# Kernel tuning notes

Measured on AMD Instinct MI355X. Metric: run time of the kernel, lower is better.

The kernel has to match this reference:

```python
import jax, jax.numpy as jnp
import numpy as np

B, N, D, H = 2, 2048, 1024, 16
HD = D // H  # 64
EPS = 1e-6


def setup_inputs() -> dict:
    key = jax.random.key(0)
    ks = jax.random.split(key, 16)
    rnd = lambda k, shp: jax.random.normal(k, shp, dtype=jnp.float32)
    w = lambda k, i, o: rnd(k, (i, o)) * 0.02  # stored as (in, out); y = x @ W
    return {
        "x": rnd(ks[0], (B, N, D)),
        "emb_B_D": rnd(ks[1], (B, D)),
        "gate": rnd(ks[2], (B, D)),
        "crossattn_emb": rnd(ks[3], (B, 128, D)),
        "rope_emb_L_1_1_D": rnd(ks[4], (N, HD)),
        "Wq1": w(ks[5], D, D), "Wq2": w(ks[6], D, D),
        "Wk1": w(ks[7], D, D), "Wk2": w(ks[8], D, D),
        "Wv": w(ks[9], D, D),
        "Wo": w(ks[10], D, D),
        "Wada1": w(ks[11], D, D),
        "Wada2": w(ks[12], D, 2 * D),
        "bada2": jnp.zeros((2 * D,), dtype=jnp.float32),
    }


def rotate_half(t):
    t1, t2 = jnp.split(t, 2, axis=-1)
    return jnp.concatenate([-t2, t1], axis=-1)


def reference(x, emb_B_D, gate, crossattn_emb, rope_emb_L_1_1_D,
              Wq1, Wq2, Wk1, Wk2, Wv, Wo, Wada1, Wada2, bada2):
    # adaLN modulation: SiLU -> Linear(no bias) -> Linear(bias)
    ada = jax.nn.silu(emb_B_D) @ Wada1 @ Wada2 + bada2          # [B, 2D]
    shift, scale = jnp.split(ada, 2, axis=1)                    # [B, D] each

    # LayerNorm (no affine) + scale/shift
    mu = jnp.mean(x, axis=-1, keepdims=True)
    var = jnp.var(x, axis=-1, keepdims=True)
    xn = (x - mu) * jax.lax.rsqrt(var + EPS)
    xn = xn * (1.0 + scale[:, None, :]) + shift[:, None, :]     # [B, N, D]

    # QKV projections (each to_q/to_k is two stacked linears, to_v one)
    q = xn @ Wq1 @ Wq2
    k = xn @ Wk1 @ Wk2
    v = xn @ Wv
    split_heads = lambda t: t.reshape(B, N, H, HD).transpose(0, 2, 1, 3)  # b h n d
    q, k, v = split_heads(q), split_heads(k), split_heads(v)

    # RoPE
    cos = jnp.cos(rope_emb_L_1_1_D)[None, None]                 # [1,1,N,HD]
    sin = jnp.sin(rope_emb_L_1_1_D)[None, None]
    q = q * cos + rotate_half(q) * sin
    k = k * cos + rotate_half(k) * sin

    # Attention
    sim = jnp.einsum("bhid,bhjd->bhij", q, k) * (HD ** -0.5)
    attn = jax.nn.softmax(sim, axis=-1)
    out = jnp.einsum("bhij,bhjd->bhid", attn, v)
    out = out.transpose(0, 2, 1, 3).reshape(B, N, D) @ Wo

    # Gated residual
    return x + gate[:, None, :] * out
```

## Files before the change

kernel.cpp:

```cpp
#include <hip/hip_runtime.h>
#include <stdint.h>
#include <math.h>

typedef unsigned short u16;
typedef __attribute__((ext_vector_type(8))) short short8;
typedef __attribute__((ext_vector_type(4))) float f32x4;
typedef __attribute__((ext_vector_type(4))) unsigned short u16x4;
typedef __attribute__((ext_vector_type(2))) unsigned int uint2v;

#define DEV static __device__ __forceinline__

DEV u16 f2bf(float f) {
    unsigned u = __builtin_bit_cast(unsigned, f);
    u = u + 0x7fffu + ((u >> 16) & 1u);
    return (u16)(u >> 16);
}
DEV float bf2f(u16 s) { return __builtin_bit_cast(float, ((unsigned)s) << 16); }
DEV unsigned pk2(float a, float b) {
    unsigned ua = __builtin_bit_cast(unsigned, a) + 0x8000u;
    unsigned ub = __builtin_bit_cast(unsigned, b) + 0x8000u;
    return (ua >> 16) | (ub & 0xffff0000u);
}
DEV float fexp2(float x) {
#if __has_builtin(__builtin_amdgcn_exp2f)
    return __builtin_amdgcn_exp2f(x);
#else
    return __expf(x * 0.69314718056f);
#endif
}

DEV void gl_lds16(const u16* g, u16* l) {
#if __has_builtin(__builtin_amdgcn_global_load_lds)
    __builtin_amdgcn_global_load_lds((const __attribute__((address_space(1))) unsigned int*)g,
                                     (__attribute__((address_space(3))) unsigned int*)l, 16, 0, 0);
#else
    *(short8*)l = *(const short8*)g;
#endif
}


__global__ __launch_bounds__(256) void k_ada1(const float* __restrict__ emb, const float* __restrict__ W,
                                              float* __restrict__ out) {
    int col = blockIdx.x * 64 + (threadIdx.x & 63);
    int b = blockIdx.y;
    int kbase = blockIdx.z * 128 + (threadIdx.x >> 6) * 32;
    float acc = 0.f;
    for (int k = kbase; k < kbase + 32; k++) {
        float e = emb[b * 1024 + k];
        float se = e / (1.f + __expf(-e));
        acc += se * W[(size_t)k * 1024 + col];
    }
    __shared__ float red[4][64];
    red[threadIdx.x >> 6][threadIdx.x & 63] = acc;
    __syncthreads();
    if (threadIdx.x < 64)
        atomicAdd(out + b * 1024 + blockIdx.x * 64 + threadIdx.x,
                  red[0][threadIdx.x] + red[1][threadIdx.x] + red[2][threadIdx.x] + red[3][threadIdx.x]);
}

__global__ __launch_bounds__(256) void k_prep(const float* s0, u16* d0, const float* s1, u16* d1,
                                              const float* s2, u16* d2, const float* s3, u16* d3,
                                              const float* s4, u16* d4, const float* s5, u16* d5,
                                              const float* __restrict__ t_ada, const float* __restrict__ Wada2,
                                              float* __restrict__ ada, const float* __restrict__ rope,
                                              float* __restrict__ cst, float* __restrict__ snt) {
    __shared__ u16 tile[64][65];
    __shared__ float red[4][64];
    if (blockIdx.z == 6) {
        int flat = blockIdx.y * 16 + blockIdx.x;
        int kq = flat >> 6;
        int rest = flat & 63;
        int b = rest >> 5, xb = rest & 31;
        int col = xb * 64 + (threadIdx.x & 63);
        int kbase = kq * 256 + (threadIdx.x >> 6) * 64;
        float acc = 0.f;
        for (int k = kbase; k < kbase + 64; k++)
            acc += t_ada[b * 1024 + k] * Wada2[(size_t)k * 2048 + col];
        red[threadIdx.x >> 6][threadIdx.x & 63] = acc;
        __syncthreads();
        if (threadIdx.x < 64)
            atomicAdd(ada + b * 2048 + xb * 64 + threadIdx.x,
                      red[0][threadIdx.x] + red[1][threadIdx.x] + red[2][threadIdx.x] + red[3][threadIdx.x]);
        return;
    }
    if (blockIdx.z == 7) {
        int flat = blockIdx.y * 16 + blockIdx.x;
        if (flat < 128) {
            int idx = flat * 1024 + threadIdx.x * 4;
            float4 rv = *(const float4*)(rope + idx);
            float4 cv, sv;
            __sincosf(rv.x, &sv.x, &cv.x);
            __sincosf(rv.y, &sv.y, &cv.y);
            __sincosf(rv.z, &sv.z, &cv.z);
            __sincosf(rv.w, &sv.w, &cv.w);
            *(float4*)(cst + idx) = cv;
            *(float4*)(snt + idx) = sv;
        }
        return;
    }
    const float* s; u16* d;
    switch (blockIdx.z) {
        case 0: s = s0; d = d0; break;
        case 1: s = s1; d = d1; break;
        case 2: s = s2; d = d2; break;
        case 3: s = s3; d = d3; break;
        case 4: s = s4; d = d4; break;
        default: s = s5; d = d5; break;
    }
    int k0 = blockIdx.x * 64, n0 = blockIdx.y * 64;
    int tx = threadIdx.x & 63, ty = threadIdx.x >> 6;
    if (blockIdx.z >= 4) {
        #pragma unroll
        for (int i = 0; i < 16; i++) {
            int kk = ty + 4 * i;
            d[(size_t)(k0 + kk) * 1024 + n0 + tx] = f2bf(s[(size_t)(k0 + kk) * 1024 + n0 + tx]);
        }
        return;
    }
    #pragma unroll
    for (int i = 0; i < 16; i++) {
        int kk = ty + 4 * i;
        tile[kk][tx] = f2bf(s[(size_t)(k0 + kk) * 1024 + n0 + tx]);
    }
    __syncthreads();
    #pragma unroll
    for (int i = 0; i < 16; i++) {
        int nn = ty + 4 * i;
        d[(size_t)(n0 + nn) * 1024 + k0 + tx] = tile[tx][nn];
    }
}

__global__ __launch_bounds__(256) void k_ln(const float* __restrict__ x, const float* __restrict__ ada,
                                            const float* __restrict__ bada2, u16* __restrict__ xn) {
    int row = blockIdx.x;
    int b = row >> 11;
    float4 v = ((const float4*)(x + (size_t)row * 1024))[threadIdx.x];
    float s = v.x + v.y + v.z + v.w;
    float ss = v.x * v.x + v.y * v.y + v.z * v.z + v.w * v.w;
    #pragma unroll
    for (int m = 1; m < 64; m <<= 1) { s += __shfl_xor(s, m, 64); ss += __shfl_xor(ss, m, 64); }
    __shared__ float red[2][4];
    int wave = threadIdx.x >> 6, lane = threadIdx.x & 63;
    if (lane == 0) { red[0][wave] = s; red[1][wave] = ss; }
    __syncthreads();
    s = red[0][0] + red[0][1] + red[0][2] + red[0][3];
    ss = red[1][0] + red[1][1] + red[1][2] + red[1][3];
    float mu = s * (1.f / 1024.f);
    float var = ss * (1.f / 1024.f) - mu * mu;
    float rs = rsqrtf(var + 1e-6f);
    int c = threadIdx.x * 4;
    const float* sh = ada + b * 2048;
    const float* sc = ada + b * 2048 + 1024;
    u16x4 r;
    r.x = f2bf((v.x - mu) * rs * (1.f + sc[c + 0] + bada2[1024 + c + 0]) + sh[c + 0] + bada2[c + 0]);
    r.y = f2bf((v.y - mu) * rs * (1.f + sc[c + 1] + bada2[1024 + c + 1]) + sh[c + 1] + bada2[c + 1]);
    r.z = f2bf((v.z - mu) * rs * (1.f + sc[c + 2] + bada2[1024 + c + 2]) + sh[c + 2] + bada2[c + 2]);
    r.w = f2bf((v.w - mu) * rs * (1.f + sc[c + 3] + bada2[1024 + c + 3]) + sh[c + 3] + bada2[c + 3]);
    *(u16x4*)(xn + (size_t)row * 1024 + c) = r;
}

template <int BM, int BN, int MODE>
DEV void gemm_core(const u16* __restrict__ A, const u16* __restrict__ Bt,
                   u16* __restrict__ Cb, float* __restrict__ Cf, u16* __restrict__ Vt,
                   const float* __restrict__ Xres, const float* __restrict__ gate,
                   const float* __restrict__ cst, const float* __restrict__ snt,
                   float scale, int Nn, int K, int m0, int n0) {
    constexpr int MI = BM / 32, NJ = BN / 32;
    constexpr int PA = BM / 64, PB = BN / 64;
    constexpr int LA = BM * 40, LB = BN * 40;
    __shared__ u16 smem[2 * (LA + LB)];
    int tid = threadIdx.x;
    int lane = tid & 63, wave = tid >> 6;
    int wm = (wave & 1) * (BM / 2), wn = (wave >> 1) * (BN / 2);
    int lr = lane & 15, quad = lane >> 4;
    f32x4 acc[MI][NJ];
    #pragma unroll
    for (int i = 0; i < MI; i++)
        #pragma unroll
        for (int j = 0; j < NJ; j++) acc[i][j] = f32x4{0.f, 0.f, 0.f, 0.f};

    int arow = tid >> 2;
    int achunk = (tid & 3) * 8;
    const u16* ap = A + (size_t)(m0 + arow) * K + achunk;
    const u16* bp = Bt + (size_t)(n0 + arow) * K + achunk;
    u16* AsL[2] = { smem, smem + LA };
    u16* BsL[2] = { smem + 2 * LA, smem + 2 * LA + LB };

    short8 ra[2][PA], rb[2][PB];
    #pragma unroll
    for (int p = 0; p < PA; p++) ra[0][p] = *(const short8*)(ap + (size_t)(64 * p) * K);
    #pragma unroll
    for (int p = 0; p < PB; p++) rb[0][p] = *(const short8*)(bp + (size_t)(64 * p) * K);
    #pragma unroll
    for (int p = 0; p < PA; p++) *(short8*)(&AsL[0][(arow + 64 * p) * 40 + achunk]) = ra[0][p];
    #pragma unroll
    for (int p = 0; p < PB; p++) *(short8*)(&BsL[0][(arow + 64 * p) * 40 + achunk]) = rb[0][p];
    #pragma unroll
    for (int p = 0; p < PA; p++) ra[1][p] = *(const short8*)(ap + 32 + (size_t)(64 * p) * K);
    #pragma unroll
    for (int p = 0; p < PB; p++) rb[1][p] = *(const short8*)(bp + 32 + (size_t)(64 * p) * K);
    __syncthreads();

    auto body = [&](int it, int cur) {
        if (it + 2 < 32) {
            int koff = (it + 2) * 32;
            #pragma unroll
            for (int p = 0; p < PA; p++) ra[cur][p] = *(const short8*)(ap + koff + (size_t)(64 * p) * K);
            #pragma unroll
            for (int p = 0; p < PB; p++) rb[cur][p] = *(const short8*)(bp + koff + (size_t)(64 * p) * K);
        }
        short8 af[MI], bfr[NJ];
        #pragma unroll
        for (int i = 0; i < MI; i++) af[i] = *(const short8*)(&AsL[cur][(wm + i * 16 + lr) * 40 + quad * 8]);
        #pragma unroll
        for (int j = 0; j < NJ; j++) bfr[j] = *(const short8*)(&BsL[cur][(wn + j * 16 + lr) * 40 + quad * 8]);
        #pragma unroll
        for (int i = 0; i < MI; i++)
            #pragma unroll
            for (int j = 0; j < NJ; j++)
                acc[i][j] = __builtin_amdgcn_mfma_f32_16x16x32_bf16(af[i], bfr[j], acc[i][j], 0, 0, 0);
        if (it + 1 < 32) {
            int nxt = cur ^ 1;
            #pragma unroll
            for (int p = 0; p < PA; p++) *(short8*)(&AsL[nxt][(arow + 64 * p) * 40 + achunk]) = ra[nxt][p];
            #pragma unroll
            for (int p = 0; p < PB; p++) *(short8*)(&BsL[nxt][(arow + 64 * p) * 40 + achunk]) = rb[nxt][p];
        }
        __syncthreads();
    };
    #pragma unroll 1
    for (int it2 = 0; it2 < 16; ++it2) {
        body(2 * it2, 0);
        body(2 * it2 + 1, 1);
    }

    if (MODE == 2) {
        if ((n0 + wn) < 2048) {
            #pragma unroll
            for (int i = 0; i < MI; i++)
                #pragma unroll
                for (int jp = 0; jp < 2; jp++)
                    #pragma unroll
                    for (int r = 0; r < 4; r++) {
                        int row = m0 + wm + i * 16 + quad * 4 + r;
                        int n = row & 2047;
                        int d1 = jp * 16 + lr;
                        float c1 = cst[n * 64 + d1],      s1 = snt[n * 64 + d1];
                        float c2 = cst[n * 64 + d1 + 32], s2 = snt[n * 64 + d1 + 32];
                        float x1 = acc[i][jp][r], x2 = acc[i][jp + 2][r];
                        Cb[(size_t)row * Nn + n0 + wn + d1]      = f2bf(x1 * c1 - x2 * s1);
                        Cb[(size_t)row * Nn + n0 + wn + d1 + 32] = f2bf(x2 * c2 + x1 * s2);
                    }
        } else {
            #pragma unroll
            for (int i = 0; i < MI; i++)
                #pragma unroll
                for (int j = 0; j < NJ; j++) {
                    u16x4 w;
                    w.x = f2bf(acc[i][j][0]); w.y = f2bf(acc[i][j][1]);
                    w.z = f2bf(acc[i][j][2]); w.w = f2bf(acc[i][j][3]);
                    *(u16x4*)(&smem[(wn + j * 16 + lr) * 132 + wm + i * 16 + quad * 4]) = w;
                }
            __syncthreads();
            int d = tid >> 1, half = tid & 1;
            int gcol = n0 - 2048 + d;
            int hv = gcol >> 6, dl = gcol & 63;
            int bb = m0 >> 11;
            int nloc = (m0 & 2047) + half * 64;
            u16* dst = Vt + ((size_t)((bb * 16 + hv) * 64 + dl)) * 2048 + nloc;
            #pragma unroll
            for (int c = 0; c < 8; c++)
                *(short8*)(dst + c * 8) = *(const short8*)(&smem[d * 132 + half * 64 + c * 8]);
        }
        return;
    }
    #pragma unroll
    for (int i = 0; i < MI; i++)
        #pragma unroll
        for (int j = 0; j < NJ; j++)
            #pragma unroll
            for (int r = 0; r < 4; r++) {
                int row = m0 + wm + i * 16 + quad * 4 + r;
                int col = n0 + wn + j * 16 + lr;
                float v = acc[i][j][r];
                if (MODE == 1) {
                    int b = row >> 11;
                    Cf[(size_t)row * Nn + col] = Xres[(size_t)row * Nn + col] + gate[b * 1024 + col] * v;
                } else {
                    Cb[(size_t)row * Nn + col] = f2bf(v * scale);
                }
            }
}

template <int BM, int BN, int MODE, int WPE>
__global__ __launch_bounds__(256, WPE) void gemm_bt(const u16* __restrict__ A, const u16* __restrict__ Bt,
                                                    u16* __restrict__ Cb, float* __restrict__ Cf,
                                                    u16* __restrict__ Vt,
                                                    const float* __restrict__ Xres, const float* __restrict__ gate,
                                                    const float* __restrict__ cst, const float* __restrict__ snt,
                                                    int Nn, int K) {
    gemm_core<BM, BN, MODE>(A, Bt, Cb, Cf, Vt, Xres, gate, cst, snt, 1.f, Nn, K,
                            blockIdx.y * BM, blockIdx.x * BN);
}

__global__ __launch_bounds__(256, 4) void gemm_fold(const u16* A0, const u16* B0, u16* C0,
                                                    const u16* A1, const u16* B1, u16* C1) {
    const u16* A = blockIdx.z ? A1 : A0;
    const u16* Bt = blockIdx.z ? B1 : B0;
    u16* C = blockIdx.z ? C1 : C0;
    float scale = blockIdx.z ? 1.0f : 0.18033688f;
    gemm_core<128, 64, 0>(A, Bt, C, nullptr, nullptr, nullptr, nullptr, nullptr, nullptr, scale,
                          1024, 1024, blockIdx.y * 128, blockIdx.x * 64);
}

__global__ __launch_bounds__(256) void k_attn(const u16* __restrict__ qkv, const u16* __restrict__ vt,
                                              u16* __restrict__ aob) {
    __shared__ u16 pool[128 * 72];
    __shared__ u16 Ks[2][64][64];
    __shared__ u16 Vs[2][64][64];
    int q0 = blockIdx.x * 128;
    int bh = blockIdx.y; int b = bh >> 4, h = bh & 15;
    int tid = threadIdx.x;
    int lane = tid & 63, wave = tid >> 6;
    int lr = lane & 15, quad = lane >> 4;
    int srow = tid >> 3, scol = (tid & 7) * 8;
    int sg = (((tid & 7) ^ (srow & 7))) * 8;
    int cc[2] = { ((quad ^ (lr & 7))) * 8, (((4 + quad) ^ (lr & 7))) * 8 };

    const u16* kp = qkv + ((size_t)(b * 2048 + srow)) * 2048 + 1024 + h * 64 + sg;
    const u16* vp = vt + ((size_t)(bh * 64 + srow)) * 2048 + sg;

    #pragma unroll
    for (int p = 0; p < 4; p++)
        gl_lds16(qkv + ((size_t)(b * 2048 + q0 + srow + 32 * p)) * 2048 + h * 64 + sg,
                 pool + (srow + 32 * p) * 64 + scol);

    short8 krA[2], vrA[2], krB[2], vrB[2];
    krA[0] = *(const short8*)(kp);               krA[1] = *(const short8*)(kp + (size_t)32 * 2048);
    vrA[0] = *(const short8*)(vp);               vrA[1] = *(const short8*)(vp + (size_t)32 * 2048);
    __syncthreads();
    short8 qf[2][2];
    #pragma unroll
    for (int rt = 0; rt < 2; rt++)
        #pragma unroll
        for (int ks = 0; ks < 2; ks++)
            qf[rt][ks] = *(const short8*)(pool + (wave * 32 + rt * 16 + lr) * 64 + cc[ks]);
    *(short8*)(&Ks[0][srow][scol])      = krA[0];
    *(short8*)(&Ks[0][srow + 32][scol]) = krA[1];
    *(short8*)(&Vs[0][srow][scol])      = vrA[0];
    *(short8*)(&Vs[0][srow + 32][scol]) = vrA[1];
    krB[0] = *(const short8*)(kp + (size_t)64 * 2048);  krB[1] = *(const short8*)(kp + (size_t)96 * 2048);
    vrB[0] = *(const short8*)(vp + 64);                 vrB[1] = *(const short8*)(vp + 64 + (size_t)32 * 2048);
    __syncthreads();

    float l_part[2] = {0.f, 0.f};
    f32x4 oacc[2][4];
    #pragma unroll
    for (int rt = 0; rt < 2; rt++)
        #pragma unroll
        for (int dt = 0; dt < 4; dt++) oacc[rt][dt] = f32x4{0.f, 0.f, 0.f, 0.f};

    auto body = [&](int it, int cur, short8 (&krF)[2], short8 (&vrF)[2],
                    short8 (&krH)[2], short8 (&vrH)[2]) {
        if (it < 30) {
            const u16* kq = kp + (size_t)(it + 2) * 64 * 2048;
            const u16* vq = vp + (it + 2) * 64;
            krF[0] = *(const short8*)(kq);  krF[1] = *(const short8*)(kq + (size_t)32 * 2048);
            vrF[0] = *(const short8*)(vq);  vrF[1] = *(const short8*)(vq + (size_t)32 * 2048);
        }
        f32x4 st[2][4];
        #pragma unroll
        for (int rt = 0; rt < 2; rt++)
            #pragma unroll
            for (int ct = 0; ct < 4; ct++) st[rt][ct] = f32x4{0.f, 0.f, 0.f, 0.f};
        #pragma unroll
        for (int ks = 0; ks < 2; ks++) {
            short8 kf[4];
            #pragma unroll
            for (int ct = 0; ct < 4; ct++)
                kf[ct] = *(const short8*)(&Ks[cur][ct * 16 + lr][cc[ks]]);
            __builtin_amdgcn_s_setprio(1);
            #pragma unroll
            for (int rt = 0; rt < 2; rt++)
                #pragma unroll
                for (int ct = 0; ct < 4; ct++)
                    st[rt][ct] = __builtin_amdgcn_mfma_f32_16x16x32_bf16(kf[ct], qf[rt][ks], st[rt][ct], 0, 0, 0);
            __builtin_amdgcn_s_setprio(0);
        }
        #pragma unroll
        for (int rt = 0; rt < 2; rt++)
            #pragma unroll
            for (int ct = 0; ct < 4; ct++) {
                float p0 = fexp2(st[rt][ct][0]);
                float p1 = fexp2(st[rt][ct][1]);
                float p2 = fexp2(st[rt][ct][2]);
                float p3 = fexp2(st[rt][ct][3]);
                l_part[rt] += (p0 + p1) + (p2 + p3);
                uint2v w; w.x = pk2(p0, p1); w.y = pk2(p2, p3);
                *(uint2v*)(pool + (wave * 32 + rt * 16 + lr) * 72 + ct * 16 + quad * 4) = w;
            }
        #pragma unroll
        for (int ks = 0; ks < 2; ks++) {
            short8 pf[2], vf[4];
            #pragma unroll
            for (int rt = 0; rt < 2; rt++)
                pf[rt] = *(const short8*)(pool + (wave * 32 + rt * 16 + lr) * 72 + ks * 32 + quad * 8);
            #pragma unroll
            for (int dt = 0; dt < 4; dt++)
                vf[dt] = *(const short8*)(&Vs[cur][dt * 16 + lr][cc[ks]]);
            __builtin_amdgcn_s_setprio(1);
            #pragma unroll
            for (int rt = 0; rt < 2; rt++)
                #pragma unroll
                for (int dt = 0; dt < 4; dt++)
                    oacc[rt][dt] = __builtin_amdgcn_mfma_f32_16x16x32_bf16(pf[rt], vf[dt], oacc[rt][dt], 0, 0, 0);
            __builtin_amdgcn_s_setprio(0);
        }
        if (it < 31) {
            int nxt = cur ^ 1;
            *(short8*)(&Ks[nxt][srow][scol])      = krH[0];
            *(short8*)(&Ks[nxt][srow + 32][scol]) = krH[1];
            *(short8*)(&Vs[nxt][srow][scol])      = vrH[0];
            *(short8*)(&Vs[nxt][srow + 32][scol]) = vrH[1];
        }
        __syncthreads();
    };

    #pragma unroll 1
    for (int it2 = 0; it2 < 16; ++it2) {
        body(2 * it2,     0, krA, vrA, krB, vrB);
        body(2 * it2 + 1, 1, krB, vrB, krA, vrA);
    }

    float linv[2][4];
    #pragma unroll
    for (int rt = 0; rt < 2; rt++) {
        float l = l_part[rt];
        l += __shfl_xor(l, 16, 64);
        l += __shfl_xor(l, 32, 64);
        #pragma unroll
        for (int r = 0; r < 4; r++)
            linv[rt][r] = 1.f / __shfl(l, quad * 4 + r, 64);
    }
    #pragma unroll
    for (int rt = 0; rt < 2; rt++)
        #pragma unroll
        for (int dt = 0; dt < 4; dt++)
            #pragma unroll
            for (int r = 0; r < 4; r++) {
                int row = q0 + wave * 32 + rt * 16 + quad * 4 + r;
                aob[((size_t)(b * 2048 + row)) * 1024 + h * 64 + dt * 16 + lr] =
                    f2bf(oacc[rt][dt][r] * linv[rt][r]);
            }
}

extern "C" void kernel_launch(void* const* d_in, const int* in_sizes, int n_in,
                              void* d_out, int out_size, void* d_ws, size_t ws_size,
                              hipStream_t stream) {
    const float* x     = (const float*)d_in[0];
    const float* emb   = (const float*)d_in[1];
    const float* gate  = (const float*)d_in[2];
    const float* rope  = (const float*)d_in[4];
    const float* Wq1   = (const float*)d_in[5];
    const float* Wq2   = (const float*)d_in[6];
    const float* Wk1   = (const float*)d_in[7];
    const float* Wk2   = (const float*)d_in[8];
    const float* Wv    = (const float*)d_in[9];
    const float* Wo    = (const float*)d_in[10];
    const float* Wada1 = (const float*)d_in[11];
    const float* Wada2 = (const float*)d_in[12];
    const float* bada2 = (const float*)d_in[13];
    float* out = (float*)d_out;

    char* ws = (char*)d_ws;
    size_t off = 0;
    auto alloc = [&](size_t bytes) { void* p = ws + off; off += (bytes + 255) & ~(size_t)255; return p; };
    float* t_ada = (float*)alloc(2048 * 4);
    float* ada   = (float*)alloc(4096 * 4);
    float* cst   = (float*)alloc((size_t)131072 * 4);
    float* snt   = (float*)alloc((size_t)131072 * 4);
    u16* xn    = (u16*)alloc((size_t)4096 * 1024 * 2);
    u16* Wq1b  = (u16*)alloc((size_t)1024 * 1024 * 2);
    u16* Wk1b  = (u16*)alloc((size_t)1024 * 1024 * 2);
    u16* Wq2t  = (u16*)alloc((size_t)1024 * 1024 * 2);
    u16* Wk2t  = (u16*)alloc((size_t)1024 * 1024 * 2);
    u16* Wot   = (u16*)alloc((size_t)1024 * 1024 * 2);
    u16* WqkvT = (u16*)alloc((size_t)3072 * 1024 * 2);
    u16* qkvb  = (u16*)alloc((size_t)4096 * 2048 * 2);
    u16* vtb   = (u16*)alloc((size_t)4096 * 1024 * 2);
    u16* aob   = (u16*)alloc((size_t)4096 * 1024 * 2);
    (void)ws_size; (void)in_sizes; (void)n_in; (void)out_size;

    hipMemsetAsync(t_ada, 0, 2048 * 4, stream);
    hipMemsetAsync(ada, 0, 4096 * 4, stream);

    k_ada1<<<dim3(16, 2, 8), 256, 0, stream>>>(emb, Wada1, t_ada);

    k_prep<<<dim3(16, 16, 8), 256, 0, stream>>>(Wq2, Wq2t, Wk2, Wk2t,
                                                Wv, WqkvT + (size_t)2048 * 1024, Wo, Wot,
                                                Wq1, Wq1b, Wk1, Wk1b,
                                                t_ada, Wada2, ada, rope, cst, snt);

    k_ln<<<4096, 256, 0, stream>>>(x, ada, bada2, xn);

    gemm_fold<<<dim3(16, 8, 2), 256, 0, stream>>>(Wq2t, Wq1b, WqkvT,
                                                  Wk2t, Wk1b, WqkvT + (size_t)1024 * 1024);

    gemm_bt<128, 128, 2, 3><<<dim3(24, 32), 256, 0, stream>>>(xn, WqkvT, qkvb, nullptr, vtb,
                                                              nullptr, nullptr, cst, snt, 2048, 1024);

    k_attn<<<dim3(16, 32), 256, 0, stream>>>(qkvb, vtb, aob);

    gemm_bt<128, 64, 1, 4><<<dim3(16, 32), 256, 0, stream>>>(aob, Wot, nullptr, out, nullptr, x, gate,
                                                             nullptr, nullptr, 1024, 1024);
}
```

Measured before the change: 265.1 us.

## Use 8 waves per attention block with 16 query rows per wave

The attention kernel now launches 512 threads per block instead of 256. Each wave handles 16 query rows rather than 32, and each thread loads one K/V chunk per tile instead of two. This raises the number of waves per block and cuts per-thread register use, which should help hide latency. In exchange, each K/V tile staged in LDS is reused by fewer rows per wave, and more threads take part in every block barrier.

```diff
diff --git a/kernel.cpp b/kernel.cpp
--- a/kernel.cpp
+++ b/kernel.cpp
@@ -313,7 +313,7 @@
                           1024, 1024, blockIdx.y * 128, blockIdx.x * 64);
 }
 
-__global__ __launch_bounds__(256) void k_attn(const u16* __restrict__ qkv, const u16* __restrict__ vt,
+__global__ __launch_bounds__(512) void k_attn(const u16* __restrict__ qkv, const u16* __restrict__ vt,
                                               u16* __restrict__ aob) {
     __shared__ u16 pool[128 * 72];
     __shared__ u16 Ks[2][64][64];
@@ -326,53 +326,43 @@
     int srow = tid >> 3, scol = (tid & 7) * 8;
     int sg = (((tid & 7) ^ (srow & 7))) * 8;
     int cc[2] = { ((quad ^ (lr & 7))) * 8, (((4 + quad) ^ (lr & 7))) * 8 };
+    int qrow = wave * 16 + lr;
 
     const u16* kp = qkv + ((size_t)(b * 2048 + srow)) * 2048 + 1024 + h * 64 + sg;
     const u16* vp = vt + ((size_t)(bh * 64 + srow)) * 2048 + sg;
 
     #pragma unroll
-    for (int p = 0; p < 4; p++)
-        gl_lds16(qkv + ((size_t)(b * 2048 + q0 + srow + 32 * p)) * 2048 + h * 64 + sg,
-                 pool + (srow + 32 * p) * 64 + scol);
-
-    short8 krA[2], vrA[2], krB[2], vrB[2];
-    krA[0] = *(const short8*)(kp);               krA[1] = *(const short8*)(kp + (size_t)32 * 2048);
-    vrA[0] = *(const short8*)(vp);               vrA[1] = *(const short8*)(vp + (size_t)32 * 2048);
-    __syncthreads();
-    short8 qf[2][2];
-    #pragma unroll
-    for (int rt = 0; rt < 2; rt++)
-        #pragma unroll
-        for (int ks = 0; ks < 2; ks++)
-            qf[rt][ks] = *(const short8*)(pool + (wave * 32 + rt * 16 + lr) * 64 + cc[ks]);
-    *(short8*)(&Ks[0][srow][scol])      = krA[0];
-    *(short8*)(&Ks[0][srow + 32][scol]) = krA[1];
-    *(short8*)(&Vs[0][srow][scol])      = vrA[0];
-    *(short8*)(&Vs[0][srow + 32][scol]) = vrA[1];
-    krB[0] = *(const short8*)(kp + (size_t)64 * 2048);  krB[1] = *(const short8*)(kp + (size_t)96 * 2048);
-    vrB[0] = *(const short8*)(vp + 64);                 vrB[1] = *(const short8*)(vp + 64 + (size_t)32 * 2048);
-    __syncthreads();
-
-    float l_part[2] = {0.f, 0.f};
-    f32x4 oacc[2][4];
-    #pragma unroll
-    for (int rt = 0; rt < 2; rt++)
-        #pragma unroll
-        for (int dt = 0; dt < 4; dt++) oacc[rt][dt] = f32x4{0.f, 0.f, 0.f, 0.f};
-
-    auto body = [&](int it, int cur, short8 (&krF)[2], short8 (&vrF)[2],
-                    short8 (&krH)[2], short8 (&vrH)[2]) {
+    for (int p = 0; p < 2; p++)
+        gl_lds16(qkv + ((size_t)(b * 2048 + q0 + srow + 64 * p)) * 2048 + h * 64 + sg,
+                 pool + (srow + 64 * p) * 64 + scol);
+
+    short8 krA, vrA, krB, vrB;
+    krA = *(const short8*)(kp);
+    vrA = *(const short8*)(vp);
+    __syncthreads();
+    short8 qf[2];
+    #pragma unroll
+    for (int ks = 0; ks < 2; ks++)
+        qf[ks] = *(const short8*)(pool + qrow * 64 + cc[ks]);
+    *(short8*)(&Ks[0][srow][scol]) = krA;
+    *(short8*)(&Vs[0][srow][scol]) = vrA;
+    krB = *(const short8*)(kp + (size_t)64 * 2048);
+    vrB = *(const short8*)(vp + 64);
+    __syncthreads();
+
+    float l_part = 0.f;
+    f32x4 oacc[4];
+    #pragma unroll
+    for (int dt = 0; dt < 4; dt++) oacc[dt] = f32x4{0.f, 0.f, 0.f, 0.f};
+
+    auto body = [&](int it, int cur, short8& krF, short8& vrF, short8& krH, short8& vrH) {
         if (it < 30) {
-            const u16* kq = kp + (size_t)(it + 2) * 64 * 2048;
-            const u16* vq = vp + (it + 2) * 64;
-            krF[0] = *(const short8*)(kq);  krF[1] = *(const short8*)(kq + (size_t)32 * 2048);
-            vrF[0] = *(const short8*)(vq);  vrF[1] = *(const short8*)(vq + (size_t)32 * 2048);
-        }
-        f32x4 st[2][4];
-        #pragma unroll
-        for (int rt = 0; rt < 2; rt++)
-            #pragma unroll
-            for (int ct = 0; ct < 4; ct++) st[rt][ct] = f32x4{0.f, 0.f, 0.f, 0.f};
+            krF = *(const short8*)(kp + (size_t)(it + 2) * 64 * 2048);
+            vrF = *(const short8*)(vp + (it + 2) * 64);
+        }
+        f32x4 st[4];
+        #pragma unroll
+        for (int ct = 0; ct < 4; ct++) st[ct] = f32x4{0.f, 0.f, 0.f, 0.f};
         #pragma unroll
         for (int ks = 0; ks < 2; ks++) {
             short8 kf[4];
@@ -381,47 +371,37 @@
                 kf[ct] = *(const short8*)(&Ks[cur][ct * 16 + lr][cc[ks]]);
             __builtin_amdgcn_s_setprio(1);
             #pragma unroll
-            for (int rt = 0; rt < 2; rt++)
-                #pragma unroll
-                for (int ct = 0; ct < 4; ct++)
-                    st[rt][ct] = __builtin_amdgcn_mfma_f32_16x16x32_bf16(kf[ct], qf[rt][ks], st[rt][ct], 0, 0, 0);
+            for (int ct = 0; ct < 4; ct++)
+                st[ct] = __builtin_amdgcn_mfma_f32_16x16x32_bf16(kf[ct], qf[ks], st[ct], 0, 0, 0);
             __builtin_amdgcn_s_setprio(0);
         }
         #pragma unroll
-        for (int rt = 0; rt < 2; rt++)
-            #pragma unroll
-            for (int ct = 0; ct < 4; ct++) {
-                float p0 = fexp2(st[rt][ct][0]);
-                float p1 = fexp2(st[rt][ct][1]);
-                float p2 = fexp2(st[rt][ct][2]);
-                float p3 = fexp2(st[rt][ct][3]);
-                l_part[rt] += (p0 + p1) + (p2 + p3);
-                uint2v w; w.x = pk2(p0, p1); w.y = pk2(p2, p3);
-                *(uint2v*)(pool + (wave * 32 + rt * 16 + lr) * 72 + ct * 16 + quad * 4) = w;
-            }
+        for (int ct = 0; ct < 4; ct++) {
+            float p0 = fexp2(st[ct][0]);
+            float p1 = fexp2(st[ct][1]);
+            float p2 = fexp2(st[ct][2]);
+            float p3 = fexp2(st[ct][3]);
+            l_part += (p0 + p1) + (p2 + p3);
+            uint2v w; w.x = pk2(p0, p1); w.y = pk2(p2, p3);
+            *(uint2v*)(pool + qrow * 72 + ct * 16 + quad * 4) = w;
+        }
         #pragma unroll
         for (int ks = 0; ks < 2; ks++) {
-            short8 pf[2], vf[4];
-            #pragma unroll
-            for (int rt = 0; rt < 2; rt++)
-                pf[rt] = *(const short8*)(pool + (wave * 32 + rt * 16 + lr) * 72 + ks * 32 + quad * 8);
+            short8 pf, vf[4];
+            pf = *(const short8*)(pool + qrow * 72 + ks * 32 + quad * 8);
             #pragma unroll
             for (int dt = 0; dt < 4; dt++)
                 vf[dt] = *(const short8*)(&Vs[cur][dt * 16 + lr][cc[ks]]);
             __builtin_amdgcn_s_setprio(1);
             #pragma unroll
-            for (int rt = 0; rt < 2; rt++)
-                #pragma unroll
-                for (int dt = 0; dt < 4; dt++)
-                    oacc[rt][dt] = __builtin_amdgcn_mfma_f32_16x16x32_bf16(pf[rt], vf[dt], oacc[rt][dt], 0, 0, 0);
+            for (int dt = 0; dt < 4; dt++)
+                oacc[dt] = __builtin_amdgcn_mfma_f32_16x16x32_bf16(pf, vf[dt], oacc[dt], 0, 0, 0);
             __builtin_amdgcn_s_setprio(0);
         }
         if (it < 31) {
             int nxt = cur ^ 1;
-            *(short8*)(&Ks[nxt][srow][scol])      = krH[0];
-            *(short8*)(&Ks[nxt][srow + 32][scol]) = krH[1];
-            *(short8*)(&Vs[nxt][srow][scol])      = vrH[0];
-            *(short8*)(&Vs[nxt][srow + 32][scol]) = vrH[1];
+            *(short8*)(&Ks[nxt][srow][scol]) = krH;
+            *(short8*)(&Vs[nxt][srow][scol]) = vrH;
         }
         __syncthreads();
     };
@@ -432,26 +412,21 @@
         body(2 * it2 + 1, 1, krB, vrB, krA, vrA);
     }
 
-    float linv[2][4];
-    #pragma unroll
-    for (int rt = 0; rt < 2; rt++) {
-        float l = l_part[rt];
-        l += __shfl_xor(l, 16, 64);
-        l += __shfl_xor(l, 32, 64);
-        #pragma unroll
-        for (int r = 0; r < 4; r++)
-            linv[rt][r] = 1.f / __shfl(l, quad * 4 + r, 64);
-    }
-    #pragma unroll
-    for (int rt = 0; rt < 2; rt++)
-        #pragma unroll
-        for (int dt = 0; dt < 4; dt++)
-            #pragma unroll
-            for (int r = 0; r < 4; r++) {
-                int row = q0 + wave * 32 + rt * 16 + quad * 4 + r;
-                aob[((size_t)(b * 2048 + row)) * 1024 + h * 64 + dt * 16 + lr] =
-                    f2bf(oacc[rt][dt][r] * linv[rt][r]);
-            }
+    float l = l_part;
+    l += __shfl_xor(l, 16, 64);
+    l += __shfl_xor(l, 32, 64);
+    float linv[4];
+    #pragma unroll
+    for (int r = 0; r < 4; r++)
+        linv[r] = 1.f / __shfl(l, quad * 4 + r, 64);
+    #pragma unroll
+    for (int dt = 0; dt < 4; dt++)
+        #pragma unroll
+        for (int r = 0; r < 4; r++) {
+            int row = q0 + wave * 16 + quad * 4 + r;
+            aob[((size_t)(b * 2048 + row)) * 1024 + h * 64 + dt * 16 + lr] =
+                f2bf(oacc[dt][r] * linv[r]);
+        }
 }
 
 extern "C" void kernel_launch(void* const* d_in, const int* in_sizes, int n_in,
@@ -509,7 +484,7 @@
     gemm_bt<128, 128, 2, 3><<<dim3(24, 32), 256, 0, stream>>>(xn, WqkvT, qkvb, nullptr, vtb,
                                                               nullptr, nullptr, cst, snt, 2048, 1024);
 
-    k_attn<<<dim3(16, 32), 256, 0, stream>>>(qkvb, vtb, aob);
+    k_attn<<<dim3(16, 32), 512, 0, stream>>>(qkvb, vtb, aob);
 
     gemm_bt<128, 64, 1, 4><<<dim3(16, 32), 256, 0, stream>>>(aob, Wot, nullptr, out, nullptr, x, gate,
                                                              nullptr, nullptr, 1024, 1024);
```

Measured after the change: 263.1 us. About the same (-0.8%).

## Split attention over key halves with 512-thread blocks and a combine kernel

Applied to the files above, without the earlier changes.

The attention kernel now gives each block 256 query rows across 8 waves, so each K/V tile is staged once and shared by more queries. It also splits the key range into two halves along a new grid z dimension. Each half writes unnormalized bf16 partial outputs and fp32 row sums to workspace. A new combine kernel adds the two partials and divides by the summed denominators. This appears to rely on softmax needing no running max, since partials are added directly. It costs an extra launch, extra global traffic, and a second bf16 rounding of the partial outputs.

```diff
diff --git a/kernel.cpp b/kernel.cpp
--- a/kernel.cpp
+++ b/kernel.cpp
@@ -313,13 +313,15 @@
                           1024, 1024, blockIdx.y * 128, blockIdx.x * 64);
 }
 
-__global__ __launch_bounds__(256) void k_attn(const u16* __restrict__ qkv, const u16* __restrict__ vt,
-                                              u16* __restrict__ aob) {
-    __shared__ u16 pool[128 * 72];
+__global__ __launch_bounds__(512) void k_attn(const u16* __restrict__ qkv, const u16* __restrict__ vt,
+                                              u16* __restrict__ dump, float* __restrict__ paL) {
+    __shared__ u16 pool[256 * 72];
     __shared__ u16 Ks[2][64][64];
     __shared__ u16 Vs[2][64][64];
-    int q0 = blockIdx.x * 128;
+    int q0 = blockIdx.x * 256;
     int bh = blockIdx.y; int b = bh >> 4, h = bh & 15;
+    int z = blockIdx.z;
+    int kbase = z * 1024;
     int tid = threadIdx.x;
     int lane = tid & 63, wave = tid >> 6;
     int lr = lane & 15, quad = lane >> 4;
@@ -327,17 +329,17 @@
     int sg = (((tid & 7) ^ (srow & 7))) * 8;
     int cc[2] = { ((quad ^ (lr & 7))) * 8, (((4 + quad) ^ (lr & 7))) * 8 };
 
-    const u16* kp = qkv + ((size_t)(b * 2048 + srow)) * 2048 + 1024 + h * 64 + sg;
-    const u16* vp = vt + ((size_t)(bh * 64 + srow)) * 2048 + sg;
+    const u16* kp = qkv + ((size_t)(b * 2048 + kbase + srow)) * 2048 + 1024 + h * 64 + sg;
+    const u16* vp = vt + ((size_t)(bh * 64 + srow)) * 2048 + kbase + sg;
 
     #pragma unroll
     for (int p = 0; p < 4; p++)
-        gl_lds16(qkv + ((size_t)(b * 2048 + q0 + srow + 32 * p)) * 2048 + h * 64 + sg,
-                 pool + (srow + 32 * p) * 64 + scol);
-
-    short8 krA[2], vrA[2], krB[2], vrB[2];
-    krA[0] = *(const short8*)(kp);               krA[1] = *(const short8*)(kp + (size_t)32 * 2048);
-    vrA[0] = *(const short8*)(vp);               vrA[1] = *(const short8*)(vp + (size_t)32 * 2048);
+        gl_lds16(qkv + ((size_t)(b * 2048 + q0 + srow + 64 * p)) * 2048 + h * 64 + sg,
+                 pool + (srow + 64 * p) * 64 + scol);
+
+    short8 krA, vrA, krB, vrB;
+    krA = *(const short8*)(kp);
+    vrA = *(const short8*)(vp);
     __syncthreads();
     short8 qf[2][2];
     #pragma unroll
@@ -345,12 +347,10 @@
         #pragma unroll
         for (int ks = 0; ks < 2; ks++)
             qf[rt][ks] = *(const short8*)(pool + (wave * 32 + rt * 16 + lr) * 64 + cc[ks]);
-    *(short8*)(&Ks[0][srow][scol])      = krA[0];
-    *(short8*)(&Ks[0][srow + 32][scol]) = krA[1];
-    *(short8*)(&Vs[0][srow][scol])      = vrA[0];
-    *(short8*)(&Vs[0][srow + 32][scol]) = vrA[1];
-    krB[0] = *(const short8*)(kp + (size_t)64 * 2048);  krB[1] = *(const short8*)(kp + (size_t)96 * 2048);
-    vrB[0] = *(const short8*)(vp + 64);                 vrB[1] = *(const short8*)(vp + 64 + (size_t)32 * 2048);
+    *(short8*)(&Ks[0][srow][scol]) = krA;
+    *(short8*)(&Vs[0][srow][scol]) = vrA;
+    krB = *(const short8*)(kp + (size_t)64 * 2048);
+    vrB = *(const short8*)(vp + 64);
     __syncthreads();
 
     float l_part[2] = {0.f, 0.f};
@@ -360,13 +360,10 @@
         #pragma unroll
         for (int dt = 0; dt < 4; dt++) oacc[rt][dt] = f32x4{0.f, 0.f, 0.f, 0.f};
 
-    auto body = [&](int it, int cur, short8 (&krF)[2], short8 (&vrF)[2],
-                    short8 (&krH)[2], short8 (&vrH)[2]) {
-        if (it < 30) {
-            const u16* kq = kp + (size_t)(it + 2) * 64 * 2048;
-            const u16* vq = vp + (it + 2) * 64;
-            krF[0] = *(const short8*)(kq);  krF[1] = *(const short8*)(kq + (size_t)32 * 2048);
-            vrF[0] = *(const short8*)(vq);  vrF[1] = *(const short8*)(vq + (size_t)32 * 2048);
+    auto body = [&](int it, int cur, short8& krF, short8& vrF, short8& krH, short8& vrH) {
+        if (it < 14) {
+            krF = *(const short8*)(kp + (size_t)(it + 2) * 64 * 2048);
+            vrF = *(const short8*)(vp + (it + 2) * 64);
         }
         f32x4 st[2][4];
         #pragma unroll
@@ -416,42 +413,72 @@
                     oacc[rt][dt] = __builtin_amdgcn_mfma_f32_16x16x32_bf16(pf[rt], vf[dt], oacc[rt][dt], 0, 0, 0);
             __builtin_amdgcn_s_setprio(0);
         }
-        if (it < 31) {
+        if (it < 15) {
             int nxt = cur ^ 1;
-            *(short8*)(&Ks[nxt][srow][scol])      = krH[0];
-            *(short8*)(&Ks[nxt][srow + 32][scol]) = krH[1];
-            *(short8*)(&Vs[nxt][srow][scol])      = vrH[0];
-            *(short8*)(&Vs[nxt][srow + 32][scol]) = vrH[1];
+            *(short8*)(&Ks[nxt][srow][scol]) = krH;
+            *(short8*)(&Vs[nxt][srow][scol]) = vrH;
         }
         __syncthreads();
     };
 
     #pragma unroll 1
-    for (int it2 = 0; it2 < 16; ++it2) {
+    for (int it2 = 0; it2 < 8; ++it2) {
         body(2 * it2,     0, krA, vrA, krB, vrB);
         body(2 * it2 + 1, 1, krB, vrB, krA, vrA);
     }
 
-    float linv[2][4];
     #pragma unroll
     for (int rt = 0; rt < 2; rt++) {
         float l = l_part[rt];
         l += __shfl_xor(l, 16, 64);
         l += __shfl_xor(l, 32, 64);
-        #pragma unroll
-        for (int r = 0; r < 4; r++)
-            linv[rt][r] = 1.f / __shfl(l, quad * 4 + r, 64);
-    }
+        if (quad == 0)
+            paL[(size_t)z * 65536 + bh * 2048 + q0 + wave * 32 + rt * 16 + lr] = l;
+    }
+    u16* dp = dump + (size_t)z * 4194304 + ((size_t)(bh * 8 + blockIdx.x) * 512 + tid) * 32;
     #pragma unroll
     for (int rt = 0; rt < 2; rt++)
         #pragma unroll
-        for (int dt = 0; dt < 4; dt++)
+        for (int dt = 0; dt < 4; dt++) {
+            u16x4 w;
+            w.x = f2bf(oacc[rt][dt][0]); w.y = f2bf(oacc[rt][dt][1]);
+            w.z = f2bf(oacc[rt][dt][2]); w.w = f2bf(oacc[rt][dt][3]);
+            *(u16x4*)(dp + rt * 16 + dt * 4) = w;
+        }
+}
+
+__global__ __launch_bounds__(512) void k_comb(const u16* __restrict__ dump, const float* __restrict__ paL,
+                                              u16* __restrict__ aob) {
+    int bx = blockIdx.x, bh = blockIdx.y;
+    int b = bh >> 4, h = bh & 15;
+    int tid = threadIdx.x;
+    int lane = tid & 63, wave = tid >> 6;
+    int lr = lane & 15, quad = lane >> 4;
+    int q0 = bx * 256;
+    const u16* d0 = dump + ((size_t)(bh * 8 + bx) * 512 + tid) * 32;
+    const u16* d1 = d0 + 4194304;
+    #pragma unroll
+    for (int rt = 0; rt < 2; rt++) {
+        float inv[4];
+        #pragma unroll
+        for (int r = 0; r < 4; r++) {
+            int row = q0 + wave * 32 + rt * 16 + quad * 4 + r;
+            float l0 = paL[bh * 2048 + row];
+            float l1 = paL[65536 + bh * 2048 + row];
+            inv[r] = 1.f / (l0 + l1);
+        }
+        #pragma unroll
+        for (int dt = 0; dt < 4; dt++) {
+            u16x4 w0 = *(const u16x4*)(d0 + rt * 16 + dt * 4);
+            u16x4 w1 = *(const u16x4*)(d1 + rt * 16 + dt * 4);
             #pragma unroll
             for (int r = 0; r < 4; r++) {
                 int row = q0 + wave * 32 + rt * 16 + quad * 4 + r;
-                aob[((size_t)(b * 2048 + row)) * 1024 + h * 64 + dt * 16 + lr] =
-                    f2bf(oacc[rt][dt][r] * linv[rt][r]);
+                float o = (bf2f(((const u16*)&w0)[r]) + bf2f(((const u16*)&w1)[r])) * inv[r];
+                aob[((size_t)(b * 2048 + row)) * 1024 + h * 64 + dt * 16 + lr] = f2bf(o);
             }
+        }
+    }
 }
 
 extern "C" void kernel_launch(void* const* d_in, const int* in_sizes, int n_in,
@@ -489,6 +516,8 @@
     u16* qkvb  = (u16*)alloc((size_t)4096 * 2048 * 2);
     u16* vtb   = (u16*)alloc((size_t)4096 * 1024 * 2);
     u16* aob   = (u16*)alloc((size_t)4096 * 1024 * 2);
+    u16* dumpO = (u16*)alloc((size_t)2 * 4194304 * 2);
+    float* paL = (float*)alloc((size_t)2 * 65536 * 4);
     (void)ws_size; (void)in_sizes; (void)n_in; (void)out_size;
 
     hipMemsetAsync(t_ada, 0, 2048 * 4, stream);
@@ -509,7 +538,8 @@
     gemm_bt<128, 128, 2, 3><<<dim3(24, 32), 256, 0, stream>>>(xn, WqkvT, qkvb, nullptr, vtb,
                                                               nullptr, nullptr, cst, snt, 2048, 1024);
 
-    k_attn<<<dim3(16, 32), 256, 0, stream>>>(qkvb, vtb, aob);
+    k_attn<<<dim3(8, 32, 2), 512, 0, stream>>>(qkvb, vtb, dumpO, paL);
+    k_comb<<<dim3(8, 32), 512, 0, stream>>>(dumpO, paL, aob);
 
     gemm_bt<128, 64, 1, 4><<<dim3(16, 32), 256, 0, stream>>>(aob, Wot, nullptr, out, nullptr, x, gate,
                                                              nullptr, nullptr, 1024, 1024);
```

After: 275.8 us. 4.0% more time.
